# Performance work log

Measured on AMD Instinct MI355X. Metric: run time of the kernel, lower is better.

The kernel has to match this reference:

```python
import jax, jax.numpy as jnp
import numpy as np

T, IN, H, OUT = 512, 1024, 2048, 1024


def setup_inputs() -> dict:
    key = jax.random.key(0)
    ks = jax.random.split(key, 13)
    s = 0.02
    return {
        "word": jax.random.normal(ks[0], (T, 1, IN), dtype=jnp.float32),
        "W_i2h1": jax.random.normal(ks[1], (H, IN), dtype=jnp.float32) * s,
        "b_i2h1": jax.random.normal(ks[2], (H,), dtype=jnp.float32) * s,
        "W_h2h1": jax.random.normal(ks[3], (H, H), dtype=jnp.float32) * s,
        "b_h2h1": jax.random.normal(ks[4], (H,), dtype=jnp.float32) * s,
        "W_h2o1": jax.random.normal(ks[5], (OUT, H), dtype=jnp.float32) * s,
        "b_h2o1": jax.random.normal(ks[6], (OUT,), dtype=jnp.float32) * s,
        "W_i2h2": jax.random.normal(ks[7], (H, H), dtype=jnp.float32) * s,
        "b_i2h2": jax.random.normal(ks[8], (H,), dtype=jnp.float32) * s,
        "W_h2h2": jax.random.normal(ks[9], (H, H), dtype=jnp.float32) * s,
        "b_h2h2": jax.random.normal(ks[10], (H,), dtype=jnp.float32) * s,
        "W_h2o2": jax.random.normal(ks[11], (OUT, H), dtype=jnp.float32) * s,
        "b_h2o2": jax.random.normal(ks[12], (OUT,), dtype=jnp.float32) * s,
    }


def reference(word, W_i2h1, b_i2h1, W_h2h1, b_h2h1, W_h2o1, b_h2o1,
              W_i2h2, b_i2h2, W_h2h2, b_h2h2, W_h2o2, b_h2o2):
    # 2-layer vanilla tanh RNN; layer2's input is layer1's hidden state.
    # layer1's h2o projection is computed-but-unused in the original module
    # (dead code), so it is omitted from the live dataflow here.
    hidden_dtype = word.dtype
    h1_0 = jnp.zeros((1, W_h2h1.shape[0]), dtype=hidden_dtype)
    h2_0 = jnp.zeros((1, W_h2h2.shape[0]), dtype=hidden_dtype)

    def step(carry, x):  # x: [1, IN]
        h1, h2 = carry
        h1 = jnp.tanh(x @ W_i2h1.T + b_i2h1 + h1 @ W_h2h1.T + b_h2h1)
        h2 = jnp.tanh(h1 @ W_i2h2.T + b_i2h2 + h2 @ W_h2h2.T + b_h2h2)
        return (h1, h2), None

    (h1, h2), _ = jax.lax.scan(step, (h1_0, h2_0), word)
    # output of the final step only
    return h2 @ W_h2o2.T + b_h2o2
```

## Files before the change

### kernel.cpp

```cpp
#include <hip/hip_runtime.h>

#define TT   512
#define DIN  1024
#define DH   2048
#define DOUT 1024

#define NWG   256
#define HALF  128
#define NTHR  512
#define NSLOT (TT + 1)

typedef unsigned int u32;
typedef unsigned long long u64;

#define SENT 0xFFFFFFFFu
__device__ u32 gR1[NSLOT * DH];
__device__ u32 gR2[NSLOT * DH];

__device__ __forceinline__ float dot4(float4 a, float4 b) {
  return a.x * b.x + a.y * b.y + a.z * b.z + a.w * b.w;
}
__device__ __forceinline__ float wave_sum(float v) {
  #pragma unroll
  for (int off = 32; off > 0; off >>= 1) v += __shfl_down(v, off, 64);
  return v;
}
__device__ __forceinline__ u32 ld_rec(const u32* p) {
  return __hip_atomic_load((u32*)p, __ATOMIC_RELAXED, __HIP_MEMORY_SCOPE_AGENT);
}
__device__ __forceinline__ void st_rec(u32* p, u32 v) {
  __hip_atomic_store(p, v, __ATOMIC_RELAXED, __HIP_MEMORY_SCOPE_AGENT);
}
__device__ __forceinline__ float fast_tanh(float x) {
  float xc = fminf(fmaxf(x, -9.0f), 9.0f);
  float e  = __expf(2.0f * xc);
  return (e - 1.0f) * __frcp_rn(e + 1.0f);
}

__device__ __forceinline__ void poll_stage(const u32* rec, float* lds, int tid) {
  u32 v0 = SENT, v1 = SENT, v2 = SENT, v3 = SENT;
  bool d0 = false, d1 = false, d2 = false, d3 = false;
  for (;;) {
    if (!d0) { v0 = ld_rec(rec + tid           ); d0 = (v0 != SENT); }
    if (!d1) { v1 = ld_rec(rec + tid +     NTHR); d1 = (v1 != SENT); }
    if (!d2) { v2 = ld_rec(rec + tid + 2 * NTHR); d2 = (v2 != SENT); }
    if (!d3) { v3 = ld_rec(rec + tid + 3 * NTHR); d3 = (v3 != SENT); }
    if (d0 & d1 & d2 & d3) break;
    __builtin_amdgcn_s_sleep(1);
  }
  lds[tid           ] = __uint_as_float(v0);
  lds[tid +     NTHR] = __uint_as_float(v1);
  lds[tid + 2 * NTHR] = __uint_as_float(v2);
  lds[tid + 3 * NTHR] = __uint_as_float(v3);
}

__device__ __forceinline__ void poll_stage2(const u32* recA, const u32* recB,
                                            float* ldsA, float* ldsB, int tid) {
  u32 a0 = SENT, a1 = SENT, a2 = SENT, a3 = SENT;
  u32 b0 = SENT, b1 = SENT, b2 = SENT, b3 = SENT;
  bool da0 = false, da1 = false, da2 = false, da3 = false;
  bool db0 = false, db1 = false, db2 = false, db3 = false;
  for (;;) {
    if (!da0) { a0 = ld_rec(recA + tid           ); da0 = (a0 != SENT); }
    if (!da1) { a1 = ld_rec(recA + tid +     NTHR); da1 = (a1 != SENT); }
    if (!da2) { a2 = ld_rec(recA + tid + 2 * NTHR); da2 = (a2 != SENT); }
    if (!da3) { a3 = ld_rec(recA + tid + 3 * NTHR); da3 = (a3 != SENT); }
    if (!db0) { b0 = ld_rec(recB + tid           ); db0 = (b0 != SENT); }
    if (!db1) { b1 = ld_rec(recB + tid +     NTHR); db1 = (b1 != SENT); }
    if (!db2) { b2 = ld_rec(recB + tid + 2 * NTHR); db2 = (b2 != SENT); }
    if (!db3) { b3 = ld_rec(recB + tid + 3 * NTHR); db3 = (b3 != SENT); }
    if (da0 & da1 & da2 & da3 & db0 & db1 & db2 & db3) break;
    __builtin_amdgcn_s_sleep(1);
  }
  ldsA[tid           ] = __uint_as_float(a0);
  ldsA[tid +     NTHR] = __uint_as_float(a1);
  ldsA[tid + 2 * NTHR] = __uint_as_float(a2);
  ldsA[tid + 3 * NTHR] = __uint_as_float(a3);
  ldsB[tid           ] = __uint_as_float(b0);
  ldsB[tid +     NTHR] = __uint_as_float(b1);
  ldsB[tid + 2 * NTHR] = __uint_as_float(b2);
  ldsB[tid + 3 * NTHR] = __uint_as_float(b3);
}

__global__ void init_kernel() {
  int i = blockIdx.x * blockDim.x + threadIdx.x;
  int n = gridDim.x * blockDim.x;
  for (int k = i; k < NSLOT * DH; k += n) {
    st_rec(&gR1[k], SENT);
    st_rec(&gR2[k], SENT);
  }
}

__global__ __launch_bounds__(NTHR, 2)
void rnn2_kernel(const float* __restrict__ X,
                 const float* __restrict__ Wa, const float* __restrict__ ba,
                 const float* __restrict__ Wb, const float* __restrict__ bb,
                 const float* __restrict__ Wc, const float* __restrict__ bc,
                 const float* __restrict__ Wd, const float* __restrict__ bd,
                 const float* __restrict__ Wo, const float* __restrict__ bo,
                 float* __restrict__ out)
{
  const int g   = blockIdx.x;
  const int tid = threadIdx.x;
  const int w   = tid >> 6;
  const int l   = tid & 63;

  __shared__ float sA[2][DH];
  __shared__ float sB[2][DH];

  if (g < HALF) {
    const int r0 = g * 16 + 2 * w, r1 = r0 + 1;
    float4 wA0[4], wA1[4], wB0[8], wB1[8], wO[8];
    {
      const float4* p0 = (const float4*)(Wa + (size_t)r0 * DIN);
      const float4* p1 = (const float4*)(Wa + (size_t)r1 * DIN);
      #pragma unroll
      for (int j = 0; j < 4; ++j) { wA0[j] = p0[l + 64 * j]; wA1[j] = p1[l + 64 * j]; }
    }
    {
      const float4* p0 = (const float4*)(Wb + (size_t)r0 * DH);
      const float4* p1 = (const float4*)(Wb + (size_t)r1 * DH);
      #pragma unroll
      for (int j = 0; j < 8; ++j) { wB0[j] = p0[l + 64 * j]; wB1[j] = p1[l + 64 * j]; }
    }
    const int orow = g * 8 + w;
    {
      const float4* p = (const float4*)(Wo + (size_t)orow * DH);
      #pragma unroll
      for (int j = 0; j < 8; ++j) wO[j] = p[l + 64 * j];
    }
    const float b1_0 = ba[r0] + bb[r0];
    const float b1_1 = ba[r1] + bb[r1];
    const float bo_r = bo[orow];

    for (int t = 1; t <= TT; ++t) {
      float a0 = 0.f, a1 = 0.f;
      {
        const float4* px = (const float4*)(X + (size_t)(t - 1) * DIN);
        #pragma unroll
        for (int j = 0; j < 4; ++j) {
          float4 x4 = px[l + 64 * j];
          a0 += dot4(wA0[j], x4);
          a1 += dot4(wA1[j], x4);
        }
      }
      if (t > 1) {
        float* buf = sA[(t - 1) & 1];
        poll_stage(gR1 + (size_t)(t - 1) * DH, buf, tid);
        __syncthreads();
        const float4* ph = (const float4*)buf;
        #pragma unroll
        for (int j = 0; j < 8; ++j) {
          float4 h4 = ph[l + 64 * j];
          a0 += dot4(wB0[j], h4);
          a1 += dot4(wB1[j], h4);
        }
      }
      a0 = wave_sum(a0); a1 = wave_sum(a1);
      if (l == 0) {
        u32* dst = gR1 + (size_t)t * DH;
        st_rec(dst + r0, __float_as_uint(fast_tanh(a0 + b1_0)));
        st_rec(dst + r1, __float_as_uint(fast_tanh(a1 + b1_1)));
      }
    }

    poll_stage(gR2 + (size_t)TT * DH, sA[0], tid);
    __syncthreads();
    {
      const float4* ph = (const float4*)sA[0];
      float acc = 0.f;
      #pragma unroll
      for (int j = 0; j < 8; ++j) acc += dot4(wO[j], ph[l + 64 * j]);
      acc = wave_sum(acc);
      if (l == 0) out[orow] = acc + bo_r;
    }
  } else {
    const int gg = g - HALF;
    const int r0 = gg * 16 + 2 * w, r1 = r0 + 1;
    float4 wC0[8], wC1[8], wD0[8], wD1[8];
    {
      const float4* p0 = (const float4*)(Wc + (size_t)r0 * DH);
      const float4* p1 = (const float4*)(Wc + (size_t)r1 * DH);
      #pragma unroll
      for (int j = 0; j < 8; ++j) { wC0[j] = p0[l + 64 * j]; wC1[j] = p1[l + 64 * j]; }
    }
    {
      const float4* p0 = (const float4*)(Wd + (size_t)r0 * DH);
      const float4* p1 = (const float4*)(Wd + (size_t)r1 * DH);
      #pragma unroll
      for (int j = 0; j < 8; ++j) { wD0[j] = p0[l + 64 * j]; wD1[j] = p1[l + 64 * j]; }
    }
    const float b2_0 = bc[r0] + bd[r0];
    const float b2_1 = bc[r1] + bd[r1];

    for (int t = 1; t <= TT; ++t) {
      float* bufA = sA[t & 1];
      float* bufB = sB[t & 1];
      if (t > 1)
        poll_stage2(gR1 + (size_t)t * DH,
                    gR2 + (size_t)(t - 1) * DH, bufA, bufB, tid);
      else
        poll_stage(gR1 + (size_t)1 * DH, bufA, tid);
      __syncthreads();

      float a0 = 0.f, a1 = 0.f;
      {
        const float4* ph = (const float4*)bufA;
        #pragma unroll
        for (int j = 0; j < 8; ++j) {
          float4 h4 = ph[l + 64 * j];
          a0 += dot4(wC0[j], h4);
          a1 += dot4(wC1[j], h4);
        }
      }
      if (t > 1) {
        const float4* ph = (const float4*)bufB;
        #pragma unroll
        for (int j = 0; j < 8; ++j) {
          float4 h4 = ph[l + 64 * j];
          a0 += dot4(wD0[j], h4);
          a1 += dot4(wD1[j], h4);
        }
      }
      a0 = wave_sum(a0); a1 = wave_sum(a1);
      if (l == 0) {
        u32* dst = gR2 + (size_t)t * DH;
        st_rec(dst + r0, __float_as_uint(fast_tanh(a0 + b2_0)));
        st_rec(dst + r1, __float_as_uint(fast_tanh(a1 + b2_1)));
      }
    }
  }
}

extern "C" void kernel_launch(void* const* d_in, const int* in_sizes, int n_in,
                              void* d_out, int out_size, void* d_ws, size_t ws_size,
                              hipStream_t stream)
{
  (void)in_sizes; (void)n_in; (void)out_size; (void)d_ws; (void)ws_size;

  const float* X  = (const float*)d_in[0];
  const float* Wa = (const float*)d_in[1];
  const float* ba = (const float*)d_in[2];
  const float* Wb = (const float*)d_in[3];
  const float* bb = (const float*)d_in[4];
  const float* Wc = (const float*)d_in[7];
  const float* bc = (const float*)d_in[8];
  const float* Wd = (const float*)d_in[9];
  const float* bd = (const float*)d_in[10];
  const float* Wo = (const float*)d_in[11];
  const float* bo = (const float*)d_in[12];
  float* out = (float*)d_out;

  init_kernel<<<dim3(1024), dim3(256), 0, stream>>>();

  void* args[] = { &X, &Wa, &ba, &Wb, &bb, &Wc, &bc, &Wd, &bd, &Wo, &bo, &out };
  (void)hipLaunchCooperativeKernel((void*)rnn2_kernel, dim3(NWG), dim3(NTHR),
                                   args, 0, stream);
}
```

Baseline: 1.594 ms.

## Pack hidden-state pairs into 64-bit flags and issue recurrence loads early

Each wave now publishes its two hidden values as one packed 64-bit atomic store, and consumers poll with two 64-bit loads per thread instead of four 32-bit ones. Layer 1 issues its h(t-1) loads before the input projection so their latency overlaps that arithmetic. Layer 2 splits its combined poll, computing the h1 part first and then waiting on the h2 slot, at the cost of an extra __syncthreads per step. The goal is shorter per-step latency in the cross-workgroup handoff on the critical path.

```diff
diff --git a/kernel.cpp b/kernel.cpp
--- a/kernel.cpp
+++ b/kernel.cpp
@@ -9,13 +9,15 @@
 #define HALF  128
 #define NTHR  512
 #define NSLOT (TT + 1)
+#define QSLOT (DH / 2)
 
 typedef unsigned int u32;
 typedef unsigned long long u64;
 
-#define SENT 0xFFFFFFFFu
-__device__ u32 gR1[NSLOT * DH];
-__device__ u32 gR2[NSLOT * DH];
+#define SENT  0xFFFFFFFFu
+#define SENT2 0xFFFFFFFFFFFFFFFFull
+__device__ u64 gR1[NSLOT * QSLOT];
+__device__ u64 gR2[NSLOT * QSLOT];
 
 __device__ __forceinline__ float dot4(float4 a, float4 b) {
   return a.x * b.x + a.y * b.y + a.z * b.z + a.w * b.w;
@@ -25,69 +27,42 @@
   for (int off = 32; off > 0; off >>= 1) v += __shfl_down(v, off, 64);
   return v;
 }
-__device__ __forceinline__ u32 ld_rec(const u32* p) {
-  return __hip_atomic_load((u32*)p, __ATOMIC_RELAXED, __HIP_MEMORY_SCOPE_AGENT);
-}
-__device__ __forceinline__ void st_rec(u32* p, u32 v) {
+__device__ __forceinline__ u64 ld64(const u64* p) {
+  return __hip_atomic_load((u64*)p, __ATOMIC_RELAXED, __HIP_MEMORY_SCOPE_AGENT);
+}
+__device__ __forceinline__ void st64(u64* p, u64 v) {
   __hip_atomic_store(p, v, __ATOMIC_RELAXED, __HIP_MEMORY_SCOPE_AGENT);
+}
+__device__ __forceinline__ bool ok2(u64 q) {
+  return ((u32)q != SENT) & ((u32)(q >> 32) != SENT);
 }
 __device__ __forceinline__ float fast_tanh(float x) {
   float xc = fminf(fmaxf(x, -9.0f), 9.0f);
   float e  = __expf(2.0f * xc);
   return (e - 1.0f) * __frcp_rn(e + 1.0f);
 }
-
-__device__ __forceinline__ void poll_stage(const u32* rec, float* lds, int tid) {
-  u32 v0 = SENT, v1 = SENT, v2 = SENT, v3 = SENT;
-  bool d0 = false, d1 = false, d2 = false, d3 = false;
-  for (;;) {
-    if (!d0) { v0 = ld_rec(rec + tid           ); d0 = (v0 != SENT); }
-    if (!d1) { v1 = ld_rec(rec + tid +     NTHR); d1 = (v1 != SENT); }
-    if (!d2) { v2 = ld_rec(rec + tid + 2 * NTHR); d2 = (v2 != SENT); }
-    if (!d3) { v3 = ld_rec(rec + tid + 3 * NTHR); d3 = (v3 != SENT); }
-    if (d0 & d1 & d2 & d3) break;
+__device__ __forceinline__ void stage4(float* lds, int tid, u64 q0, u64 q1) {
+  ((float4*)lds)[tid] = make_float4(
+      __uint_as_float((u32)q0), __uint_as_float((u32)(q0 >> 32)),
+      __uint_as_float((u32)q1), __uint_as_float((u32)(q1 >> 32)));
+}
+
+__device__ __forceinline__ void poll_stage(const u64* slot, float* lds, int tid) {
+  const u64* p = slot + 2 * (size_t)tid;
+  u64 q0 = ld64(p), q1 = ld64(p + 1);
+  while (!(ok2(q0) & ok2(q1))) {
     __builtin_amdgcn_s_sleep(1);
+    q0 = ld64(p); q1 = ld64(p + 1);
   }
-  lds[tid           ] = __uint_as_float(v0);
-  lds[tid +     NTHR] = __uint_as_float(v1);
-  lds[tid + 2 * NTHR] = __uint_as_float(v2);
-  lds[tid + 3 * NTHR] = __uint_as_float(v3);
-}
-
-__device__ __forceinline__ void poll_stage2(const u32* recA, const u32* recB,
-                                            float* ldsA, float* ldsB, int tid) {
-  u32 a0 = SENT, a1 = SENT, a2 = SENT, a3 = SENT;
-  u32 b0 = SENT, b1 = SENT, b2 = SENT, b3 = SENT;
-  bool da0 = false, da1 = false, da2 = false, da3 = false;
-  bool db0 = false, db1 = false, db2 = false, db3 = false;
-  for (;;) {
-    if (!da0) { a0 = ld_rec(recA + tid           ); da0 = (a0 != SENT); }
-    if (!da1) { a1 = ld_rec(recA + tid +     NTHR); da1 = (a1 != SENT); }
-    if (!da2) { a2 = ld_rec(recA + tid + 2 * NTHR); da2 = (a2 != SENT); }
-    if (!da3) { a3 = ld_rec(recA + tid + 3 * NTHR); da3 = (a3 != SENT); }
-    if (!db0) { b0 = ld_rec(recB + tid           ); db0 = (b0 != SENT); }
-    if (!db1) { b1 = ld_rec(recB + tid +     NTHR); db1 = (b1 != SENT); }
-    if (!db2) { b2 = ld_rec(recB + tid + 2 * NTHR); db2 = (b2 != SENT); }
-    if (!db3) { b3 = ld_rec(recB + tid + 3 * NTHR); db3 = (b3 != SENT); }
-    if (da0 & da1 & da2 & da3 & db0 & db1 & db2 & db3) break;
-    __builtin_amdgcn_s_sleep(1);
-  }
-  ldsA[tid           ] = __uint_as_float(a0);
-  ldsA[tid +     NTHR] = __uint_as_float(a1);
-  ldsA[tid + 2 * NTHR] = __uint_as_float(a2);
-  ldsA[tid + 3 * NTHR] = __uint_as_float(a3);
-  ldsB[tid           ] = __uint_as_float(b0);
-  ldsB[tid +     NTHR] = __uint_as_float(b1);
-  ldsB[tid + 2 * NTHR] = __uint_as_float(b2);
-  ldsB[tid + 3 * NTHR] = __uint_as_float(b3);
+  stage4(lds, tid, q0, q1);
 }
 
 __global__ void init_kernel() {
   int i = blockIdx.x * blockDim.x + threadIdx.x;
   int n = gridDim.x * blockDim.x;
-  for (int k = i; k < NSLOT * DH; k += n) {
-    st_rec(&gR1[k], SENT);
-    st_rec(&gR2[k], SENT);
+  for (int k = i; k < NSLOT * QSLOT; k += n) {
+    st64(&gR1[k], SENT2);
+    st64(&gR2[k], SENT2);
   }
 }
 
@@ -110,6 +85,7 @@
 
   if (g < HALF) {
     const int r0 = g * 16 + 2 * w, r1 = r0 + 1;
+    const int qidx = 8 * g + w;
     float4 wA0[4], wA1[4], wB0[8], wB1[8], wO[8];
     {
       const float4* p0 = (const float4*)(Wa + (size_t)r0 * DIN);
@@ -134,6 +110,10 @@
     const float bo_r = bo[orow];
 
     for (int t = 1; t <= TT; ++t) {
+      const u64* pp = gR1 + (size_t)(t - 1) * QSLOT + 2 * (size_t)tid;
+      u64 q0 = 0, q1 = 0;
+      if (t > 1) { q0 = ld64(pp); q1 = ld64(pp + 1); }
+
       float a0 = 0.f, a1 = 0.f;
       {
         const float4* px = (const float4*)(X + (size_t)(t - 1) * DIN);
@@ -144,9 +124,14 @@
           a1 += dot4(wA1[j], x4);
         }
       }
+
       if (t > 1) {
+        while (!(ok2(q0) & ok2(q1))) {
+          __builtin_amdgcn_s_sleep(1);
+          q0 = ld64(pp); q1 = ld64(pp + 1);
+        }
         float* buf = sA[(t - 1) & 1];
-        poll_stage(gR1 + (size_t)(t - 1) * DH, buf, tid);
+        stage4(buf, tid, q0, q1);
         __syncthreads();
         const float4* ph = (const float4*)buf;
         #pragma unroll
@@ -158,13 +143,13 @@
       }
       a0 = wave_sum(a0); a1 = wave_sum(a1);
       if (l == 0) {
-        u32* dst = gR1 + (size_t)t * DH;
-        st_rec(dst + r0, __float_as_uint(fast_tanh(a0 + b1_0)));
-        st_rec(dst + r1, __float_as_uint(fast_tanh(a1 + b1_1)));
-      }
-    }
-
-    poll_stage(gR2 + (size_t)TT * DH, sA[0], tid);
+        u64 pr = ((u64)__float_as_uint(fast_tanh(a1 + b1_1)) << 32)
+               |  (u64)__float_as_uint(fast_tanh(a0 + b1_0));
+        st64(gR1 + (size_t)t * QSLOT + qidx, pr);
+      }
+    }
+
+    poll_stage(gR2 + (size_t)TT * QSLOT, sA[0], tid);
     __syncthreads();
     {
       const float4* ph = (const float4*)sA[0];
@@ -177,6 +162,7 @@
   } else {
     const int gg = g - HALF;
     const int r0 = gg * 16 + 2 * w, r1 = r0 + 1;
+    const int qidx = 8 * gg + w;
     float4 wC0[8], wC1[8], wD0[8], wD1[8];
     {
       const float4* p0 = (const float4*)(Wc + (size_t)r0 * DH);
@@ -194,13 +180,13 @@
     const float b2_1 = bc[r1] + bd[r1];
 
     for (int t = 1; t <= TT; ++t) {
+      const u64* pb = gR2 + (size_t)(t - 1) * QSLOT + 2 * (size_t)tid;
+      u64 qb0 = 0, qb1 = 0;
+      if (t > 1) { qb0 = ld64(pb); qb1 = ld64(pb + 1); }
+
       float* bufA = sA[t & 1];
       float* bufB = sB[t & 1];
-      if (t > 1)
-        poll_stage2(gR1 + (size_t)t * DH,
-                    gR2 + (size_t)(t - 1) * DH, bufA, bufB, tid);
-      else
-        poll_stage(gR1 + (size_t)1 * DH, bufA, tid);
+      poll_stage(gR1 + (size_t)t * QSLOT, bufA, tid);
       __syncthreads();
 
       float a0 = 0.f, a1 = 0.f;
@@ -214,6 +200,12 @@
         }
       }
       if (t > 1) {
+        while (!(ok2(qb0) & ok2(qb1))) {
+          __builtin_amdgcn_s_sleep(1);
+          qb0 = ld64(pb); qb1 = ld64(pb + 1);
+        }
+        stage4(bufB, tid, qb0, qb1);
+        __syncthreads();
         const float4* ph = (const float4*)bufB;
         #pragma unroll
         for (int j = 0; j < 8; ++j) {
@@ -224,9 +216,9 @@
       }
       a0 = wave_sum(a0); a1 = wave_sum(a1);
       if (l == 0) {
-        u32* dst = gR2 + (size_t)t * DH;
-        st_rec(dst + r0, __float_as_uint(fast_tanh(a0 + b2_0)));
-        st_rec(dst + r1, __float_as_uint(fast_tanh(a1 + b2_1)));
+        u64 pr = ((u64)__float_as_uint(fast_tanh(a1 + b2_1)) << 32)
+               |  (u64)__float_as_uint(fast_tanh(a0 + b2_0));
+        st64(gR2 + (size_t)t * QSLOT + qidx, pr);
       }
     }
   }
```

Result: slower. 2.415 ms (+51.5%).
